# Kernel tuning notes

Hardware: AMD Instinct MI355X
Metric: run time of the kernel (lower is better)

The kernel has to match this reference:

```python
import jax, jax.numpy as jnp
from jax import lax
import numpy as np

VGG_C = 512
INNER = 32


def _conv3x3(x, w, b):
    # x: [B,C,H,W], w: [O,I,3,3], padding=1 (SAME)
    y = lax.conv_general_dilated(x, w, (1, 1), 'SAME',
                                 dimension_numbers=('NCHW', 'OIHW', 'NCHW'))
    return y + b[None, :, None, None]


def _predict_filter(style, cw, cb, fw, fb):
    # FilterPredictor_S: conv 512->32, global mean pool, FC 32 -> 9*32*32
    s = _conv3x3(style, cw, cb)                     # [B,32,H,W]
    pooled = s.mean(axis=(2, 3))                    # [B,32]
    f = pooled @ fw.T + fb                          # [B,9216]
    return f.reshape(-1, INNER, INNER, 3, 3)        # [B,outC,inC,3,3]


def _apply_filter(x, filt):
    # per-sample dynamic 3x3 conv: x [B,32,H,W], filt [B,32,32,3,3]
    def one(xi, wi):
        return lax.conv_general_dilated(xi[None], wi, (1, 1), 'SAME',
                                        dimension_numbers=('NCHW', 'OIHW', 'NCHW'))[0]
    return jax.vmap(one)(x, filt)


def setup_inputs() -> dict:
    key = jax.random.key(0)
    ks = jax.random.split(key, 16)
    B, H, W = 8, 64, 64
    sc = 0.02
    d = {
        'content': jax.random.normal(ks[0], (B, VGG_C, H, W), jnp.float32),
        'style': jax.random.normal(ks[1], (B, VGG_C, H, W), jnp.float32),
        'ds_w': jax.random.normal(ks[2], (INNER, VGG_C, 3, 3), jnp.float32) * sc,
        'ds_b': jnp.zeros((INNER,), jnp.float32),
        'up_w': jax.random.normal(ks[3], (VGG_C, INNER, 3, 3), jnp.float32) * sc,
        'up_b': jnp.zeros((VGG_C,), jnp.float32),
        'f1_cw': jax.random.normal(ks[4], (INNER, VGG_C, 3, 3), jnp.float32) * sc,
        'f1_cb': jnp.zeros((INNER,), jnp.float32),
        'f1_fw': jax.random.normal(ks[5], (9 * INNER * INNER, INNER), jnp.float32) * sc,
        'f1_fb': jnp.zeros((9 * INNER * INNER,), jnp.float32),
        'f2_cw': jax.random.normal(ks[6], (INNER, VGG_C, 3, 3), jnp.float32) * sc,
        'f2_cb': jnp.zeros((INNER,), jnp.float32),
        'f2_fw': jax.random.normal(ks[7], (9 * INNER * INNER, INNER), jnp.float32) * sc,
        'f2_fb': jnp.zeros((9 * INNER * INNER,), jnp.float32),
    }
    return d


def reference(content, style, ds_w, ds_b, up_w, up_b,
              f1_cw, f1_cb, f1_fw, f1_fb,
              f2_cw, f2_cb, f2_fw, f2_fb):
    c = _conv3x3(content, ds_w, ds_b)                       # [B,32,H,W]
    filt1 = _predict_filter(style, f1_cw, f1_cb, f1_fw, f1_fb)
    c = _apply_filter(c, filt1)
    c = jnp.where(c >= 0, c, 0.2 * c)                       # LeakyReLU(0.2)
    filt2 = _predict_filter(style, f2_cw, f2_cb, f2_fw, f2_fb)
    c = _apply_filter(c, filt2)
    return content + _conv3x3(c, up_w, up_b)
```

## Files before the change

kernel.cpp:

```cpp
#include <hip/hip_runtime.h>
#include <hip/hip_bf16.h>

#define NB 8
#define NC 512
#define HW 4096
#define INNER 32

typedef unsigned short u16;
typedef unsigned int u32;
typedef __attribute__((ext_vector_type(8))) short bf16x8;
typedef __attribute__((ext_vector_type(4))) float f32x4;

__device__ __forceinline__ float b2f(u16 u) {
    union { u32 a; float f; } z;
    z.a = ((u32)u) << 16;
    return z.f;
}

__device__ __forceinline__ u16 f2b(float v) {
    u32 x = __float_as_uint(v);
    return (u16)((x + 0x7fffu + ((x >> 16) & 1u)) >> 16);
}

__device__ __forceinline__ float ldin(const void* p, int idx, int isf32) {
    if (isf32) return ((const float*)p)[idx];
    return b2f(((const u16*)p)[idx]);
}

__device__ __forceinline__ void gld_lds16(const void* g, void* l) {
    __builtin_amdgcn_global_load_lds(
        (const __attribute__((address_space(1))) unsigned int*)g,
        (__attribute__((address_space(3))) unsigned int*)l, 16, 0, 0);
}

__device__ __forceinline__ int resolve_isf32(int hisf, const void* content) {
    if (hisf >= 0) return hisf;
    int lane = threadIdx.x & 63;
    u16 u = ((const u16*)content)[lane * 2048];
    int e = (u >> 7) & 0xff;
    unsigned long long m = __ballot(e >= 100 && e <= 150);
    return (__popcll(m) < 32) ? 1 : 0;
}


__device__ __forceinline__ void role_style(int bc, const void* style, float* S,
                                           int isf32, float* smf) {
    int base = bc * HW;
    int tid = threadIdx.x;
    float t = 0.f, top = 0.f, bot = 0.f, lft = 0.f, rgt = 0.f;
    for (int e = tid; e < HW; e += 256) {
        float v = ldin(style, base + e, isf32);
        int h = e >> 6, w = e & 63;
        t += v;
        top += (h == 0)  ? v : 0.f;
        bot += (h == 63) ? v : 0.f;
        lft += (w == 0)  ? v : 0.f;
        rgt += (w == 63) ? v : 0.f;
    }
#pragma unroll
    for (int off = 32; off > 0; off >>= 1) {
        t   += __shfl_down(t, off);
        top += __shfl_down(top, off);
        bot += __shfl_down(bot, off);
        lft += __shfl_down(lft, off);
        rgt += __shfl_down(rgt, off);
    }
    int wave = tid >> 6;
    if ((tid & 63) == 0) {
        smf[wave * 5 + 0] = t; smf[wave * 5 + 1] = top; smf[wave * 5 + 2] = bot;
        smf[wave * 5 + 3] = lft; smf[wave * 5 + 4] = rgt;
    }
    __syncthreads();
    if (tid == 0) {
        t   = smf[0] + smf[5] + smf[10] + smf[15];
        top = smf[1] + smf[6] + smf[11] + smf[16];
        bot = smf[2] + smf[7] + smf[12] + smf[17];
        lft = smf[3] + smf[8] + smf[13] + smf[18];
        rgt = smf[4] + smf[9] + smf[14] + smf[19];
        float c00 = ldin(style, base + 0,    isf32);
        float c0W = ldin(style, base + 63,   isf32);
        float cH0 = ldin(style, base + 4032, isf32);
        float cHW = ldin(style, base + 4095, isf32);
        float* o = S + bc * 9;
        o[0] = t - bot - rgt + cHW;
        o[1] = t - bot;
        o[2] = t - bot - lft + cH0;
        o[3] = t - rgt;
        o[4] = t;
        o[5] = t - lft;
        o[6] = t - top - rgt + c0W;
        o[7] = t - top;
        o[8] = t - top - lft + c00;
    }
}

__device__ __forceinline__ void role_transform(int ridx, const void* content,
        u16* cT, int bstart, int isf32, float* lds) {
    int h  = ridx & 63;
    int ci = (ridx >> 6) & 15;
    int b4 = ridx >> 10;
    int tid = threadIdx.x;
    size_t gbase = ((size_t)(bstart + b4) * NC + ci * 32) * HW + (size_t)h * 64;
    if (isf32) {
#pragma unroll
        for (int k = 0; k < 2; k++) {
            int q = tid + k * 256;
            int c = q >> 4, w0 = (q & 15) * 4;
            float4 v = *(const float4*)((const float*)content + gbase + (size_t)c * HW + w0);
            lds[c * 65 + w0 + 0] = v.x;
            lds[c * 65 + w0 + 1] = v.y;
            lds[c * 65 + w0 + 2] = v.z;
            lds[c * 65 + w0 + 3] = v.w;
        }
    } else {
        int c = tid >> 3, w0 = (tid & 7) * 8;
        uint4 v = *(const uint4*)((const u16*)content + gbase + (size_t)c * HW + w0);
        lds[c * 65 + w0 + 0] = b2f((u16)(v.x & 0xffffu));
        lds[c * 65 + w0 + 1] = b2f((u16)(v.x >> 16));
        lds[c * 65 + w0 + 2] = b2f((u16)(v.y & 0xffffu));
        lds[c * 65 + w0 + 3] = b2f((u16)(v.y >> 16));
        lds[c * 65 + w0 + 4] = b2f((u16)(v.z & 0xffffu));
        lds[c * 65 + w0 + 5] = b2f((u16)(v.z >> 16));
        lds[c * 65 + w0 + 6] = b2f((u16)(v.w & 0xffffu));
        lds[c * 65 + w0 + 7] = b2f((u16)(v.w >> 16));
    }
    __syncthreads();
    u32* out = (u32*)(cT + ((size_t)(b4 * 16 + ci) * 4096 + h * 64) * 32);
#pragma unroll
    for (int k = 0; k < 4; k++) {
        int j = tid + k * 256;
        int w = j >> 4, cpair = j & 15;
        int key = (w + 1) & 3;
        int p0 = cpair << 1;
        int lc = (((p0 >> 3) ^ key) << 3) | (p0 & 7);
        u32 v = (u32)f2b(lds[lc * 65 + w]) | ((u32)f2b(lds[(lc + 1) * 65 + w]) << 16);
        out[j] = v;
    }
}

__device__ __forceinline__ void role_prep_wdown(int ridx, const void* dsw,
        u16* Bp, int isf32) {
    int idx = ridx * 256 + threadIdx.x;
    int e = idx & 7, l = (idx >> 3) & 63, nf = (idx >> 9) & 1;
    int cb = (idx >> 10) & 15, t9 = idx >> 14;
    int oc = nf * 16 + (l & 15);
    int c = cb * 32 + (l >> 4) * 8 + e;
    Bp[idx] = f2b(ldin(dsw, (oc * NC + c) * 9 + t9, isf32));
}

__device__ __forceinline__ void role_prep_wup(int ridx, const void* upw,
        u16* B2p, int isf32) {
    int idx = ridx * 256 + threadIdx.x;
    int e = idx & 7, l = (idx >> 3) & 63, nfo = (idx >> 9) & 31, t9 = idx >> 14;
    int oc = nfo * 16 + (l & 15);
    int ic = (l >> 4) * 8 + e;
    B2p[idx] = f2b(ldin(upw, (oc * INNER + ic) * 9 + t9, isf32));
}

__device__ __forceinline__ void role_fc(int ridx, const float* pooled,
        const void* fw1, const void* fb1, const void* fw2, const void* fb2,
        u16* fpack, int isf32, float* p) {
    int set = ridx / 288;
    int rr = ridx - set * 288;
    int b = rr / 36;
    int chunk = rr - b * 36;
    int row = chunk * 256 + threadIdx.x;
    const void* fw = set ? fw2 : fw1;
    const void* fb = set ? fb2 : fb1;
    if (threadIdx.x < 32) p[threadIdx.x] = pooled[(set * NB + b) * 32 + threadIdx.x];
    __syncthreads();
    float acc = ldin(fb, row, isf32);
    if (isf32) {
        const float* fwf = (const float*)fw + row * 32;
#pragma unroll
        for (int j = 0; j < 32; j++) acc += fwf[j] * p[j];
    } else {
        const u32* w32 = (const u32*)((const u16*)fw + row * 32);
#pragma unroll
        for (int j = 0; j < 16; j++) {
            u32 u = w32[j];
            acc += b2f((u16)(u & 0xffffu)) * p[2 * j];
            acc += b2f((u16)(u >> 16)) * p[2 * j + 1];
        }
    }
    int oc = row / 288;
    int rem = row - oc * 288;
    int ic = rem / 9;
    int t9 = rem - ic * 9;
    int l = (oc & 15) | ((ic >> 3) << 4);
    int e = ic & 7;
    int nf = oc >> 4;
    fpack[((((set * NB + b) * 9 + t9) * 2 + nf) * 64 + l) * 8 + e] = f2b(acc);
}

__device__ __forceinline__ void role_conv_down(int x, const u16* cT,
        const u16* Bp, const void* dsb, u16* c0T, int bstart, int isf32,
        u16* lds) {
    u32* lds32 = (u32*)lds;
    int b4 = x >> 6, row = x & 63;
    int b = bstart + b4;
    int tid = threadIdx.x, lane = tid & 63;
    int wid = __builtin_amdgcn_readfirstlane(tid >> 6);
    for (int i = tid; i < 3 * 66 * 16; i += 256) lds32[i] = 0u;
    __syncthreads();

    int m = lane & 15, g = lane >> 4;
    int wbase = wid * 16;
    f32x4 acc0 = {0.f, 0.f, 0.f, 0.f}, acc1 = {0.f, 0.f, 0.f, 0.f};

    for (int ci = 0; ci < 16; ci++) {
        if (ci) __syncthreads();
        const u16* sp = cT + ((size_t)(b4 * 16 + ci) * 4096) * 32;
#pragma unroll
        for (int r = 0; r < 3; r++) {
            int gh = row + r - 1;
            if (gh >= 0 && gh < 64)
                gld_lds16(sp + (size_t)gh * 2048 + tid * 8,
                          (char*)lds + (r * 66 + 1) * 64 + wid * 1024);
        }
        __syncthreads();
#pragma unroll
        for (int t9 = 0; t9 < 9; t9++) {
            int dh = t9 / 3, dw = t9 - dh * 3;
            int wi = wbase + m + dw;
            bf16x8 a = *(const bf16x8*)(lds + ((dh * 66 + wi) * 32 + ((g ^ (wi & 3)) * 8)));
            bf16x8 b0 = ((const bf16x8*)Bp)[((t9 * 16 + ci) * 2 + 0) * 64 + lane];
            bf16x8 b1 = ((const bf16x8*)Bp)[((t9 * 16 + ci) * 2 + 1) * 64 + lane];
            acc0 = __builtin_amdgcn_mfma_f32_16x16x32_bf16(a, b0, acc0, 0, 0, 0);
            acc1 = __builtin_amdgcn_mfma_f32_16x16x32_bf16(a, b1, acc1, 0, 0, 0);
        }
    }
    float bia0 = ldin(dsb, m, isf32);
    float bia1 = ldin(dsb, 16 + m, isf32);
    size_t obase = ((size_t)b * 4096 + row * 64) * 32;
    int pix0 = wbase + g * 4;
#pragma unroll
    for (int r = 0; r < 4; r++) {
        int w = pix0 + r;
        int key = (w + 1) & 3;
        int p0 = (((m >> 3) ^ key) << 3) | (m & 7);
        int p1 = ((((16 + m) >> 3) ^ key) << 3) | (m & 7);
        c0T[obase + (size_t)w * 32 + p0] = f2b(acc0[r] + bia0);
        c0T[obase + (size_t)w * 32 + p1] = f2b(acc1[r] + bia1);
    }
}

__device__ __forceinline__ void role_pooled(int p, const float* S,
        const void* cw1, const void* cb1, const void* cw2, const void* cb2,
        float* pooled, int isf32) {
    int tid = threadIdx.x;
    int pair = p * 4 + (tid >> 6);
    int set = pair >> 8;
    int rem = pair & 255;
    int b = rem >> 5;
    int o = rem & 31;
    const void* cw = set ? cw2 : cw1;
    const void* cb = set ? cb2 : cb1;
    int lane = tid & 63;
    float acc = 0.f;
    const float* Sb = S + b * NC * 9;
    int wbase = o * NC * 9;
    for (int c = lane; c < NC; c += 64) {
#pragma unroll
        for (int k = 0; k < 9; k++)
            acc += Sb[c * 9 + k] * ldin(cw, wbase + c * 9 + k, isf32);
    }
#pragma unroll
    for (int off = 32; off > 0; off >>= 1) acc += __shfl_down(acc, off);
    if (lane == 0)
        pooled[(set * NB + b) * INNER + o] = acc * (1.0f / 4096.0f) + ldin(cb, o, isf32);
}


__global__ __launch_bounds__(256) void k_front(
        const void* __restrict__ style, float* __restrict__ S, int nStyle,
        const void* __restrict__ content, u16* __restrict__ cT, int bstart, int nT,
        const void* __restrict__ dsw, u16* __restrict__ Bp,
        const void* __restrict__ upw, u16* __restrict__ B2p, int nPrep,
        const float* __restrict__ pooled,
        const void* __restrict__ fw1, const void* __restrict__ fb1,
        const void* __restrict__ fw2, const void* __restrict__ fb2,
        u16* __restrict__ fpack, int hisf) {
    __shared__ float smf[32 * 65];
    int isf32 = resolve_isf32(hisf, content);
    int x = blockIdx.x;
    if (x < nStyle) { role_style(x, style, S, isf32, smf); return; }
    x -= nStyle;
    if (x < nT) { role_transform(x, content, cT, bstart, isf32, smf); return; }
    x -= nT;
    if (x < nPrep) { role_prep_wdown(x, dsw, Bp, isf32); return; }
    x -= nPrep;
    if (x < nPrep) { role_prep_wup(x, upw, B2p, isf32); return; }
    x -= nPrep;
    role_fc(x, pooled, fw1, fb1, fw2, fb2, fpack, isf32, smf);
}

__global__ __launch_bounds__(256) void k_mid(
        const u16* __restrict__ cT, const u16* __restrict__ Bp,
        const void* __restrict__ dsb, u16* __restrict__ c0T, int bstart, int nCD,
        const float* __restrict__ S,
        const void* __restrict__ cw1, const void* __restrict__ cb1,
        const void* __restrict__ cw2, const void* __restrict__ cb2,
        float* __restrict__ pooled, const void* __restrict__ content, int hisf) {
    __shared__ u16 lds[3 * 66 * 32];
    int isf32 = resolve_isf32(hisf, content);
    int x = blockIdx.x;
    if (x < nCD) { role_conv_down(x, cT, Bp, dsb, c0T, bstart, isf32, lds); return; }
    role_pooled(x - nCD, S, cw1, cb1, cw2, cb2, pooled, isf32);
}

__global__ __launch_bounds__(256) void k_apply(const u16* __restrict__ srcT,
        const u16* __restrict__ fpack, u16* __restrict__ dstT, int lrelu) {
    int b = blockIdx.x >> 6, row = blockIdx.x & 63;
    int tid = threadIdx.x, lane = tid & 63;
    int wid = __builtin_amdgcn_readfirstlane(tid >> 6);
    __shared__ u16 lds[3 * 66 * 32];
    u32* lds32 = (u32*)lds;
    for (int i = tid; i < 96; i += 256) {
        int r = i >> 5, side = (i >> 4) & 1, cpr = i & 15;
        lds32[(r * 66 + side * 65) * 16 + cpr] = 0u;
    }
    const u16* sp = srcT + (size_t)b * 64 * 64 * 32;
    for (int r = 0; r < 3; r++) {
        int gh = row + r - 1;
        u32 ldsoff = (u32)(r * 66 + 1) * 64 + (u32)wid * 1024;
        if (gh >= 0 && gh < 64) {
            gld_lds16(sp + (size_t)gh * 2048 + tid * 8, (char*)lds + ldsoff);
        } else {
            int4 z = make_int4(0, 0, 0, 0);
            *(int4*)((char*)lds + ldsoff + (u32)lane * 16) = z;
        }
    }
    __syncthreads();

    int m = lane & 15, g = lane >> 4, wbase = wid * 16;
    f32x4 acc0 = {0.f, 0.f, 0.f, 0.f}, acc1 = {0.f, 0.f, 0.f, 0.f};
    const bf16x8* FB = (const bf16x8*)fpack + (size_t)b * 1152;
#pragma unroll
    for (int t9 = 0; t9 < 9; t9++) {
        int dh = t9 / 3, dw = t9 - dh * 3;
        int wi = wbase + m + dw;
        bf16x8 a = *(const bf16x8*)(lds + ((dh * 66 + wi) * 32 + ((g ^ (wi & 3)) * 8)));
        bf16x8 b0 = FB[(t9 * 2 + 0) * 64 + lane];
        bf16x8 b1 = FB[(t9 * 2 + 1) * 64 + lane];
        acc0 = __builtin_amdgcn_mfma_f32_16x16x32_bf16(a, b0, acc0, 0, 0, 0);
        acc1 = __builtin_amdgcn_mfma_f32_16x16x32_bf16(a, b1, acc1, 0, 0, 0);
    }
    size_t obase = ((size_t)(b * 64 + row) * 64) * 32;
    int pix0 = wbase + g * 4;
#pragma unroll
    for (int r = 0; r < 4; r++) {
        float v0 = acc0[r], v1 = acc1[r];
        if (lrelu) {
            v0 = (v0 >= 0.f) ? v0 : 0.2f * v0;
            v1 = (v1 >= 0.f) ? v1 : 0.2f * v1;
        }
        int w = pix0 + r;
        int key = (w + 1) & 3;
        int p0 = (((m >> 3) ^ key) << 3) | (m & 7);
        int p1 = ((((16 + m) >> 3) ^ key) << 3) | (m & 7);
        dstT[obase + (size_t)w * 32 + p0] = f2b(v0);
        dstT[obase + (size_t)w * 32 + p1] = f2b(v1);
    }
}

__global__ __launch_bounds__(256) void k_conv_up(const u16* __restrict__ c2T,
        const u16* __restrict__ B2p, const void* __restrict__ upb,
        const void* __restrict__ content, void* __restrict__ outv, int hisf) {
    int isf32 = resolve_isf32(hisf, content);
    int b = blockIdx.x >> 6, row = blockIdx.x & 63;
    int nq = blockIdx.y;
    int tid = threadIdx.x, lane = tid & 63;
    int wid = __builtin_amdgcn_readfirstlane(tid >> 6);
    __shared__ char smem[64 * 68 * 4] __attribute__((aligned(16)));
    u16* lds = (u16*)smem;
    u32* lds32 = (u32*)smem;
    for (int i = tid; i < 96; i += 256) {
        int r = i >> 5, side = (i >> 4) & 1, cpr = i & 15;
        lds32[(r * 66 + side * 65) * 16 + cpr] = 0u;
    }
    const u16* sp = c2T + (size_t)b * 64 * 64 * 32;
    for (int r = 0; r < 3; r++) {
        int gh = row + r - 1;
        u32 ldsoff = (u32)(r * 66 + 1) * 64 + (u32)wid * 1024;
        if (gh >= 0 && gh < 64) {
            gld_lds16(sp + (size_t)gh * 2048 + tid * 8, (char*)lds + ldsoff);
        } else {
            int4 z = make_int4(0, 0, 0, 0);
            *(int4*)((char*)lds + ldsoff + (u32)lane * 16) = z;
        }
    }
    __syncthreads();

    int m = lane & 15, g = lane >> 4, wbase = wid * 16;
    f32x4 acc[8];
#pragma unroll
    for (int i = 0; i < 8; i++) acc[i] = (f32x4){0.f, 0.f, 0.f, 0.f};
#pragma unroll
    for (int t9 = 0; t9 < 9; t9++) {
        int dh = t9 / 3, dw = t9 - dh * 3;
        int wi = wbase + m + dw;
        bf16x8 a = *(const bf16x8*)(lds + ((dh * 66 + wi) * 32 + ((g ^ (wi & 3)) * 8)));
#pragma unroll
        for (int nfl = 0; nfl < 8; nfl++) {
            bf16x8 bw = ((const bf16x8*)B2p)[(t9 * 32 + nq * 8 + nfl) * 64 + lane];
            acc[nfl] = __builtin_amdgcn_mfma_f32_16x16x32_bf16(a, bw, acc[nfl], 0, 0, 0);
        }
    }

    int pix0 = wbase + g * 4;
    float* fl = (float*)smem;
    int ocl2 = tid >> 4;
    int px0 = (tid & 15) * 4;
    __syncthreads();
#pragma unroll
    for (int hf = 0; hf < 2; hf++) {
        if (hf) __syncthreads();
#pragma unroll
        for (int nf = 0; nf < 4; nf++) {
            int ocl = nf * 16 + m;
            *(f32x4*)(fl + ocl * 68 + pix0) = acc[hf * 4 + nf];
        }
        __syncthreads();
#pragma unroll
        for (int p = 0; p < 4; p++) {
            int ocl = p * 16 + ocl2;
            int oc = nq * 128 + hf * 64 + ocl;
            float bias = ldin(upb, oc, isf32);
            f32x4 v4 = *(const f32x4*)(fl + ocl * 68 + px0);
            size_t idx = ((size_t)b * NC + oc) * HW + (size_t)row * 64 + px0;
            if (isf32) {
                f32x4 rsd = *(const f32x4*)((const float*)content + idx);
                f32x4 ov;
#pragma unroll
                for (int r = 0; r < 4; r++) ov[r] = v4[r] + bias + rsd[r];
                *(f32x4*)((float*)outv + idx) = ov;
            } else {
                ushort4 rv = *(const ushort4*)((const u16*)content + idx);
                ushort4 ov;
                ov.x = f2b(v4[0] + bias + b2f(rv.x));
                ov.y = f2b(v4[1] + bias + b2f(rv.y));
                ov.z = f2b(v4[2] + bias + b2f(rv.z));
                ov.w = f2b(v4[3] + bias + b2f(rv.w));
                *(ushort4*)((u16*)outv + idx) = ov;
            }
        }
    }
}

extern "C" void kernel_launch(void* const* d_in, const int* in_sizes, int n_in,
                              void* d_out, int out_size, void* d_ws, size_t ws_size,
                              hipStream_t stream) {
    const void* content = d_in[0];
    const void* style   = d_in[1];
    const void* ds_w    = d_in[2];
    const void* ds_b    = d_in[3];
    const void* up_w    = d_in[4];
    const void* up_b    = d_in[5];
    const void* f1_cw   = d_in[6];
    const void* f1_cb   = d_in[7];
    const void* f1_fw   = d_in[8];
    const void* f1_fb   = d_in[9];
    const void* f2_cw   = d_in[10];
    const void* f2_cb   = d_in[11];
    const void* f2_fw   = d_in[12];
    const void* f2_fb   = d_in[13];

    int hisf = -1;
    if (in_sizes && n_in >= 1) {
        if (in_sizes[0] == NB * NC * HW * 4) hisf = 1;
        else if (in_sizes[0] == NB * NC * HW * 2) hisf = 0;
    }

    const size_t SZ_PACK = 294912;
    const size_t SZ_CT2  = 2097152;
    const size_t REQ_WS  = 3 * SZ_CT2 + 3 * SZ_PACK + 147456 * 4 + 2048 + 64;

    if (ws_size >= REQ_WS) {
        char* w = (char*)d_ws;
        u16*   B2pack = (u16*)w;                 w += SZ_PACK;
        u16*   c2T    = (u16*)w;                 w += SZ_CT2;
        u16*   c0T    = (u16*)w;                 w += SZ_CT2;
        u16*   c1T    = (u16*)w;                 w += SZ_CT2;
        u16*   Bpack  = (u16*)w;                 w += SZ_PACK;
        u16*   fpack  = (u16*)w;                 w += SZ_PACK;
        float* S      = (float*)w;               w += 147456 * 4;
        float* pooled = (float*)w;
        u16*   cT     = (u16*)d_out;

        k_front<<<4096 + 8192 + 2 * 576, 256, 0, stream>>>(
            style, S, 4096, content, cT, 0, 8192,
            ds_w, Bpack, up_w, B2pack, 576,
            pooled, f1_fw, f1_fb, f2_fw, f2_fb, fpack, hisf);
        k_mid<<<512 + 128, 256, 0, stream>>>(
            cT, Bpack, ds_b, c0T, 0, 512,
            S, f1_cw, f1_cb, f2_cw, f2_cb, pooled, content, hisf);
        k_front<<<576, 256, 0, stream>>>(
            style, S, 0, content, cT, 0, 0,
            ds_w, Bpack, up_w, B2pack, 0,
            pooled, f1_fw, f1_fb, f2_fw, f2_fb, fpack, hisf);
        k_apply<<<NB * 64, 256, 0, stream>>>(c0T, fpack, c1T, 1);
        k_apply<<<NB * 64, 256, 0, stream>>>(c1T, fpack + NB * 9216, c2T, 0);
        k_conv_up<<<dim3(NB * 64, 4), 256, 0, stream>>>(c2T, B2pack, up_b,
                                                        content, d_out, hisf);
    } else {
        float* S      = (float*)d_out;
        float* pooled = S + 36864;
        u16*   fpack  = (u16*)(pooled + 512);
        u16*   Bpack  = fpack + 147456;
        u16*   c0T    = Bpack + 147456;
        u16*   c1T    = c0T + 1048576;
        u16*   cTh    = c1T + 1048576;
        u16*   B2pack = (u16*)d_ws;
        u16*   c2T    = B2pack + 147456;

        k_front<<<4096 + 4096 + 2 * 576, 256, 0, stream>>>(
            style, S, 4096, content, cTh, 0, 4096,
            ds_w, Bpack, up_w, B2pack, 576,
            pooled, f1_fw, f1_fb, f2_fw, f2_fb, fpack, hisf);
        k_mid<<<256 + 128, 256, 0, stream>>>(
            cTh, Bpack, ds_b, c0T, 0, 256,
            S, f1_cw, f1_cb, f2_cw, f2_cb, pooled, content, hisf);
        k_front<<<4096 + 576, 256, 0, stream>>>(
            style, S, 0, content, cTh, 4, 4096,
            ds_w, Bpack, up_w, B2pack, 0,
            pooled, f1_fw, f1_fb, f2_fw, f2_fb, fpack, hisf);
        k_mid<<<256, 256, 0, stream>>>(
            cTh, Bpack, ds_b, c0T, 4, 256,
            S, f1_cw, f1_cb, f2_cw, f2_cb, pooled, content, hisf);
        k_apply<<<NB * 64, 256, 0, stream>>>(c0T, fpack, c1T, 1);
        k_apply<<<NB * 64, 256, 0, stream>>>(c1T, fpack + NB * 9216, c2T, 0);
        k_conv_up<<<dim3(NB * 64, 4), 256, 0, stream>>>(c2T, B2pack, up_b,
                                                        content, d_out, hisf);
    }
}
```

Measured before the change: 283.6 us.

## Fuse style pooling conv into style blocks via atomics, drop extra FC launch

Each style block now projects its nine shifted-window sums through both predictor conv weights and atomically accumulates into a raw pooled buffer. This removes the S intermediate and the separate pooled role, and moves the FC role into k_mid, which cuts one kernel launch. The style reduction is vectorised, and the transform role now handles two rows per block to halve its block count. In exchange it adds a memset and atomic contention, and the float summation order now varies from run to run.

```diff
diff --git a/kernel.cpp b/kernel.cpp
--- a/kernel.cpp
+++ b/kernel.cpp
@@ -43,19 +43,45 @@
 }
 
 
-__device__ __forceinline__ void role_style(int bc, const void* style, float* S,
-                                           int isf32, float* smf) {
+__device__ __forceinline__ void role_style(int bc, const void* style,
+        const void* cw1, const void* cw2, float* pooled_raw,
+        int isf32, float* smf) {
+    int b = bc >> 9, c = bc & 511;
     int base = bc * HW;
     int tid = threadIdx.x;
     float t = 0.f, top = 0.f, bot = 0.f, lft = 0.f, rgt = 0.f;
-    for (int e = tid; e < HW; e += 256) {
-        float v = ldin(style, base + e, isf32);
-        int h = e >> 6, w = e & 63;
-        t += v;
-        top += (h == 0)  ? v : 0.f;
-        bot += (h == 63) ? v : 0.f;
-        lft += (w == 0)  ? v : 0.f;
-        rgt += (w == 63) ? v : 0.f;
+    if (isf32) {
+        const float4* sp = (const float4*)((const float*)style + base);
+#pragma unroll
+        for (int k = 0; k < 4; k++) {
+            int q = tid + k * 256;
+            float4 v = sp[q];
+            float s4 = (v.x + v.y) + (v.z + v.w);
+            int h = q >> 4, w0 = (q & 15) * 4;
+            t += s4;
+            if (h == 0)   top += s4;
+            if (h == 63)  bot += s4;
+            if (w0 == 0)  lft += v.x;
+            if (w0 == 60) rgt += v.w;
+        }
+    } else {
+        const uint4* sp = (const uint4*)((const u16*)style + base);
+#pragma unroll
+        for (int k = 0; k < 2; k++) {
+            int q = tid + k * 256;
+            uint4 v = sp[q];
+            float e0 = b2f((u16)(v.x & 0xffffu)), e1 = b2f((u16)(v.x >> 16));
+            float e2 = b2f((u16)(v.y & 0xffffu)), e3 = b2f((u16)(v.y >> 16));
+            float e4 = b2f((u16)(v.z & 0xffffu)), e5 = b2f((u16)(v.z >> 16));
+            float e6 = b2f((u16)(v.w & 0xffffu)), e7 = b2f((u16)(v.w >> 16));
+            float s8 = ((e0 + e1) + (e2 + e3)) + ((e4 + e5) + (e6 + e7));
+            int h = q >> 3, w0 = (q & 7) * 8;
+            t += s8;
+            if (h == 0)   top += s8;
+            if (h == 63)  bot += s8;
+            if (w0 == 0)  lft += e0;
+            if (w0 == 56) rgt += e7;
+        }
     }
 #pragma unroll
     for (int off = 32; off > 0; off >>= 1) {
@@ -67,74 +93,95 @@
     }
     int wave = tid >> 6;
     if ((tid & 63) == 0) {
-        smf[wave * 5 + 0] = t; smf[wave * 5 + 1] = top; smf[wave * 5 + 2] = bot;
-        smf[wave * 5 + 3] = lft; smf[wave * 5 + 4] = rgt;
+        smf[20 + wave * 5 + 0] = t;   smf[20 + wave * 5 + 1] = top;
+        smf[20 + wave * 5 + 2] = bot; smf[20 + wave * 5 + 3] = lft;
+        smf[20 + wave * 5 + 4] = rgt;
     }
     __syncthreads();
     if (tid == 0) {
-        t   = smf[0] + smf[5] + smf[10] + smf[15];
-        top = smf[1] + smf[6] + smf[11] + smf[16];
-        bot = smf[2] + smf[7] + smf[12] + smf[17];
-        lft = smf[3] + smf[8] + smf[13] + smf[18];
-        rgt = smf[4] + smf[9] + smf[14] + smf[19];
+        t   = smf[20] + smf[25] + smf[30] + smf[35];
+        top = smf[21] + smf[26] + smf[31] + smf[36];
+        bot = smf[22] + smf[27] + smf[32] + smf[37];
+        lft = smf[23] + smf[28] + smf[33] + smf[38];
+        rgt = smf[24] + smf[29] + smf[34] + smf[39];
         float c00 = ldin(style, base + 0,    isf32);
         float c0W = ldin(style, base + 63,   isf32);
         float cH0 = ldin(style, base + 4032, isf32);
         float cHW = ldin(style, base + 4095, isf32);
-        float* o = S + bc * 9;
-        o[0] = t - bot - rgt + cHW;
-        o[1] = t - bot;
-        o[2] = t - bot - lft + cH0;
-        o[3] = t - rgt;
-        o[4] = t;
-        o[5] = t - lft;
-        o[6] = t - top - rgt + c0W;
-        o[7] = t - top;
-        o[8] = t - top - lft + c00;
+        smf[0] = t - bot - rgt + cHW;
+        smf[1] = t - bot;
+        smf[2] = t - bot - lft + cH0;
+        smf[3] = t - rgt;
+        smf[4] = t;
+        smf[5] = t - lft;
+        smf[6] = t - top - rgt + c0W;
+        smf[7] = t - top;
+        smf[8] = t - top - lft + c00;
+    }
+    __syncthreads();
+    if (tid < 64) {
+        int set = tid >> 5, o = tid & 31;
+        const void* cw = set ? cw2 : cw1;
+        int wb = (o * NC + c) * 9;
+        float acc = 0.f;
+#pragma unroll
+        for (int k = 0; k < 9; k++) acc += ldin(cw, wb + k, isf32) * smf[k];
+        atomicAdd(&pooled_raw[(set * NB + b) * 32 + o], acc);
     }
 }
 
 __device__ __forceinline__ void role_transform(int ridx, const void* content,
         u16* cT, int bstart, int isf32, float* lds) {
-    int h  = ridx & 63;
-    int ci = (ridx >> 6) & 15;
-    int b4 = ridx >> 10;
+    int hp = ridx & 31;
+    int ci = (ridx >> 5) & 15;
+    int b4 = ridx >> 9;
     int tid = threadIdx.x;
-    size_t gbase = ((size_t)(bstart + b4) * NC + ci * 32) * HW + (size_t)h * 64;
+    size_t gbase = ((size_t)(bstart + b4) * NC + ci * 32) * HW + (size_t)hp * 128;
     if (isf32) {
 #pragma unroll
-        for (int k = 0; k < 2; k++) {
-            int q = tid + k * 256;
-            int c = q >> 4, w0 = (q & 15) * 4;
-            float4 v = *(const float4*)((const float*)content + gbase + (size_t)c * HW + w0);
-            lds[c * 65 + w0 + 0] = v.x;
-            lds[c * 65 + w0 + 1] = v.y;
-            lds[c * 65 + w0 + 2] = v.z;
-            lds[c * 65 + w0 + 3] = v.w;
-        }
+        for (int r2 = 0; r2 < 2; r2++)
+#pragma unroll
+            for (int k = 0; k < 2; k++) {
+                int q = tid + k * 256;
+                int c = q >> 4, w0 = (q & 15) * 4;
+                float4 v = *(const float4*)((const float*)content
+                            + gbase + (size_t)c * HW + r2 * 64 + w0);
+                float* dst = lds + r2 * 2080 + c * 65 + w0;
+                dst[0] = v.x; dst[1] = v.y; dst[2] = v.z; dst[3] = v.w;
+            }
     } else {
-        int c = tid >> 3, w0 = (tid & 7) * 8;
-        uint4 v = *(const uint4*)((const u16*)content + gbase + (size_t)c * HW + w0);
-        lds[c * 65 + w0 + 0] = b2f((u16)(v.x & 0xffffu));
-        lds[c * 65 + w0 + 1] = b2f((u16)(v.x >> 16));
-        lds[c * 65 + w0 + 2] = b2f((u16)(v.y & 0xffffu));
-        lds[c * 65 + w0 + 3] = b2f((u16)(v.y >> 16));
-        lds[c * 65 + w0 + 4] = b2f((u16)(v.z & 0xffffu));
-        lds[c * 65 + w0 + 5] = b2f((u16)(v.z >> 16));
-        lds[c * 65 + w0 + 6] = b2f((u16)(v.w & 0xffffu));
-        lds[c * 65 + w0 + 7] = b2f((u16)(v.w >> 16));
-    }
-    __syncthreads();
-    u32* out = (u32*)(cT + ((size_t)(b4 * 16 + ci) * 4096 + h * 64) * 32);
-#pragma unroll
-    for (int k = 0; k < 4; k++) {
-        int j = tid + k * 256;
-        int w = j >> 4, cpair = j & 15;
-        int key = (w + 1) & 3;
-        int p0 = cpair << 1;
-        int lc = (((p0 >> 3) ^ key) << 3) | (p0 & 7);
-        u32 v = (u32)f2b(lds[lc * 65 + w]) | ((u32)f2b(lds[(lc + 1) * 65 + w]) << 16);
-        out[j] = v;
+#pragma unroll
+        for (int r2 = 0; r2 < 2; r2++) {
+            int c = tid >> 3, w0 = (tid & 7) * 8;
+            uint4 v = *(const uint4*)((const u16*)content
+                        + gbase + (size_t)c * HW + r2 * 64 + w0);
+            float* dst = lds + r2 * 2080 + c * 65 + w0;
+            dst[0] = b2f((u16)(v.x & 0xffffu));
+            dst[1] = b2f((u16)(v.x >> 16));
+            dst[2] = b2f((u16)(v.y & 0xffffu));
+            dst[3] = b2f((u16)(v.y >> 16));
+            dst[4] = b2f((u16)(v.z & 0xffffu));
+            dst[5] = b2f((u16)(v.z >> 16));
+            dst[6] = b2f((u16)(v.w & 0xffffu));
+            dst[7] = b2f((u16)(v.w >> 16));
+        }
+    }
+    __syncthreads();
+#pragma unroll
+    for (int r2 = 0; r2 < 2; r2++) {
+        u32* out = (u32*)(cT + ((size_t)(b4 * 16 + ci) * 4096
+                                + (hp * 2 + r2) * 64) * 32);
+        const float* src = lds + r2 * 2080;
+#pragma unroll
+        for (int k = 0; k < 4; k++) {
+            int j = tid + k * 256;
+            int w = j >> 4, cpair = j & 15;
+            int key = (w + 1) & 3;
+            int p0 = cpair << 1;
+            int lc = (((p0 >> 3) ^ key) << 3) | (p0 & 7);
+            out[j] = (u32)f2b(src[lc * 65 + w])
+                   | ((u32)f2b(src[(lc + 1) * 65 + w]) << 16);
+        }
     }
 }
 
@@ -157,7 +204,8 @@
     B2p[idx] = f2b(ldin(upw, (oc * INNER + ic) * 9 + t9, isf32));
 }
 
-__device__ __forceinline__ void role_fc(int ridx, const float* pooled,
+__device__ __forceinline__ void role_fc(int ridx, const float* pooled_raw,
+        const void* cbf1, const void* cbf2,
         const void* fw1, const void* fb1, const void* fw2, const void* fb2,
         u16* fpack, int isf32, float* p) {
     int set = ridx / 288;
@@ -167,7 +215,10 @@
     int row = chunk * 256 + threadIdx.x;
     const void* fw = set ? fw2 : fw1;
     const void* fb = set ? fb2 : fb1;
-    if (threadIdx.x < 32) p[threadIdx.x] = pooled[(set * NB + b) * 32 + threadIdx.x];
+    if (threadIdx.x < 32)
+        p[threadIdx.x] = pooled_raw[(set * NB + b) * 32 + threadIdx.x]
+                           * (1.0f / 4096.0f)
+                       + ldin(set ? cbf2 : cbf1, threadIdx.x, isf32);
     __syncthreads();
     float acc = ldin(fb, row, isf32);
     if (isf32) {
@@ -245,68 +296,41 @@
     }
 }
 
-__device__ __forceinline__ void role_pooled(int p, const float* S,
-        const void* cw1, const void* cb1, const void* cw2, const void* cb2,
-        float* pooled, int isf32) {
-    int tid = threadIdx.x;
-    int pair = p * 4 + (tid >> 6);
-    int set = pair >> 8;
-    int rem = pair & 255;
-    int b = rem >> 5;
-    int o = rem & 31;
-    const void* cw = set ? cw2 : cw1;
-    const void* cb = set ? cb2 : cb1;
-    int lane = tid & 63;
-    float acc = 0.f;
-    const float* Sb = S + b * NC * 9;
-    int wbase = o * NC * 9;
-    for (int c = lane; c < NC; c += 64) {
-#pragma unroll
-        for (int k = 0; k < 9; k++)
-            acc += Sb[c * 9 + k] * ldin(cw, wbase + c * 9 + k, isf32);
-    }
-#pragma unroll
-    for (int off = 32; off > 0; off >>= 1) acc += __shfl_down(acc, off);
-    if (lane == 0)
-        pooled[(set * NB + b) * INNER + o] = acc * (1.0f / 4096.0f) + ldin(cb, o, isf32);
-}
-
 
 __global__ __launch_bounds__(256) void k_front(
-        const void* __restrict__ style, float* __restrict__ S, int nStyle,
+        const void* __restrict__ style,
+        const void* __restrict__ cw1, const void* __restrict__ cw2,
+        float* __restrict__ pooled_raw, int nStyle,
         const void* __restrict__ content, u16* __restrict__ cT, int bstart, int nT,
         const void* __restrict__ dsw, u16* __restrict__ Bp,
         const void* __restrict__ upw, u16* __restrict__ B2p, int nPrep,
-        const float* __restrict__ pooled,
-        const void* __restrict__ fw1, const void* __restrict__ fb1,
-        const void* __restrict__ fw2, const void* __restrict__ fb2,
-        u16* __restrict__ fpack, int hisf) {
-    __shared__ float smf[32 * 65];
+        int hisf) {
+    __shared__ float smf[2 * 2080];
     int isf32 = resolve_isf32(hisf, content);
     int x = blockIdx.x;
-    if (x < nStyle) { role_style(x, style, S, isf32, smf); return; }
+    if (x < nStyle) { role_style(x, style, cw1, cw2, pooled_raw, isf32, smf); return; }
     x -= nStyle;
     if (x < nT) { role_transform(x, content, cT, bstart, isf32, smf); return; }
     x -= nT;
     if (x < nPrep) { role_prep_wdown(x, dsw, Bp, isf32); return; }
     x -= nPrep;
-    if (x < nPrep) { role_prep_wup(x, upw, B2p, isf32); return; }
-    x -= nPrep;
-    role_fc(x, pooled, fw1, fb1, fw2, fb2, fpack, isf32, smf);
+    role_prep_wup(x, upw, B2p, isf32);
 }
 
 __global__ __launch_bounds__(256) void k_mid(
         const u16* __restrict__ cT, const u16* __restrict__ Bp,
         const void* __restrict__ dsb, u16* __restrict__ c0T, int bstart, int nCD,
-        const float* __restrict__ S,
-        const void* __restrict__ cw1, const void* __restrict__ cb1,
-        const void* __restrict__ cw2, const void* __restrict__ cb2,
-        float* __restrict__ pooled, const void* __restrict__ content, int hisf) {
+        const float* __restrict__ pooled_raw,
+        const void* __restrict__ cbf1, const void* __restrict__ cbf2,
+        const void* __restrict__ fw1, const void* __restrict__ fb1,
+        const void* __restrict__ fw2, const void* __restrict__ fb2,
+        u16* __restrict__ fpack, const void* __restrict__ content, int hisf) {
     __shared__ u16 lds[3 * 66 * 32];
     int isf32 = resolve_isf32(hisf, content);
     int x = blockIdx.x;
     if (x < nCD) { role_conv_down(x, cT, Bp, dsb, c0T, bstart, isf32, lds); return; }
-    role_pooled(x - nCD, S, cw1, cb1, cw2, cb2, pooled, isf32);
+    role_fc(x - nCD, pooled_raw, cbf1, cbf2, fw1, fb1, fw2, fb2, fpack,
+            isf32, (float*)lds);
 }
 
 __global__ __launch_bounds__(256) void k_apply(const u16* __restrict__ srcT,
@@ -474,7 +498,7 @@
 
     const size_t SZ_PACK = 294912;
     const size_t SZ_CT2  = 2097152;
-    const size_t REQ_WS  = 3 * SZ_CT2 + 3 * SZ_PACK + 147456 * 4 + 2048 + 64;
+    const size_t REQ_WS  = 3 * SZ_CT2 + 3 * SZ_PACK + 2048 + 64;
 
     if (ws_size >= REQ_WS) {
         char* w = (char*)d_ws;
@@ -484,29 +508,25 @@
         u16*   c1T    = (u16*)w;                 w += SZ_CT2;
         u16*   Bpack  = (u16*)w;                 w += SZ_PACK;
         u16*   fpack  = (u16*)w;                 w += SZ_PACK;
-        float* S      = (float*)w;               w += 147456 * 4;
-        float* pooled = (float*)w;
+        float* pooled_raw = (float*)w;
         u16*   cT     = (u16*)d_out;
 
-        k_front<<<4096 + 8192 + 2 * 576, 256, 0, stream>>>(
-            style, S, 4096, content, cT, 0, 8192,
-            ds_w, Bpack, up_w, B2pack, 576,
-            pooled, f1_fw, f1_fb, f2_fw, f2_fb, fpack, hisf);
-        k_mid<<<512 + 128, 256, 0, stream>>>(
+        hipMemsetAsync(pooled_raw, 0, 2 * NB * 32 * 4, stream);
+        k_front<<<4096 + 4096 + 2 * 576, 256, 0, stream>>>(
+            style, f1_cw, f2_cw, pooled_raw, 4096,
+            content, cT, 0, 4096,
+            ds_w, Bpack, up_w, B2pack, 576, hisf);
+        k_mid<<<512 + 576, 256, 0, stream>>>(
             cT, Bpack, ds_b, c0T, 0, 512,
-            S, f1_cw, f1_cb, f2_cw, f2_cb, pooled, content, hisf);
-        k_front<<<576, 256, 0, stream>>>(
-            style, S, 0, content, cT, 0, 0,
-            ds_w, Bpack, up_w, B2pack, 0,
-            pooled, f1_fw, f1_fb, f2_fw, f2_fb, fpack, hisf);
+            pooled_raw, f1_cb, f2_cb,
+            f1_fw, f1_fb, f2_fw, f2_fb, fpack, content, hisf);
         k_apply<<<NB * 64, 256, 0, stream>>>(c0T, fpack, c1T, 1);
         k_apply<<<NB * 64, 256, 0, stream>>>(c1T, fpack + NB * 9216, c2T, 0);
         k_conv_up<<<dim3(NB * 64, 4), 256, 0, stream>>>(c2T, B2pack, up_b,
                                                         content, d_out, hisf);
     } else {
-        float* S      = (float*)d_out;
-        float* pooled = S + 36864;
-        u16*   fpack  = (u16*)(pooled + 512);
+        float* pooled_raw = (float*)d_out;
+        u16*   fpack  = (u16*)(pooled_raw + 512);
         u16*   Bpack  = fpack + 147456;
         u16*   c0T    = Bpack + 147456;
         u16*   c1T    = c0T + 1048576;
@@ -514,20 +534,23 @@
         u16*   B2pack = (u16*)d_ws;
         u16*   c2T    = B2pack + 147456;
 
-        k_front<<<4096 + 4096 + 2 * 576, 256, 0, stream>>>(
-            style, S, 4096, content, cTh, 0, 4096,
-            ds_w, Bpack, up_w, B2pack, 576,
-            pooled, f1_fw, f1_fb, f2_fw, f2_fb, fpack, hisf);
-        k_mid<<<256 + 128, 256, 0, stream>>>(
+        hipMemsetAsync(pooled_raw, 0, 2 * NB * 32 * 4, stream);
+        k_front<<<4096 + 2048 + 2 * 576, 256, 0, stream>>>(
+            style, f1_cw, f2_cw, pooled_raw, 4096,
+            content, cTh, 0, 2048,
+            ds_w, Bpack, up_w, B2pack, 576, hisf);
+        k_mid<<<256 + 576, 256, 0, stream>>>(
             cTh, Bpack, ds_b, c0T, 0, 256,
-            S, f1_cw, f1_cb, f2_cw, f2_cb, pooled, content, hisf);
-        k_front<<<4096 + 576, 256, 0, stream>>>(
-            style, S, 0, content, cTh, 4, 4096,
-            ds_w, Bpack, up_w, B2pack, 0,
-            pooled, f1_fw, f1_fb, f2_fw, f2_fb, fpack, hisf);
+            pooled_raw, f1_cb, f2_cb,
+            f1_fw, f1_fb, f2_fw, f2_fb, fpack, content, hisf);
+        k_front<<<2048, 256, 0, stream>>>(
+            style, f1_cw, f2_cw, pooled_raw, 0,
+            content, cTh, 4, 2048,
+            ds_w, Bpack, up_w, B2pack, 0, hisf);
         k_mid<<<256, 256, 0, stream>>>(
             cTh, Bpack, ds_b, c0T, 4, 256,
-            S, f1_cw, f1_cb, f2_cw, f2_cb, pooled, content, hisf);
+            pooled_raw, f1_cb, f2_cb,
+            f1_fw, f1_fb, f2_fw, f2_fb, fpack, content, hisf);
         k_apply<<<NB * 64, 256, 0, stream>>>(c0T, fpack, c1T, 1);
         k_apply<<<NB * 64, 256, 0, stream>>>(c1T, fpack + NB * 9216, c2T, 0);
         k_conv_up<<<dim3(NB * 64, 4), 256, 0, stream>>>(c2T, B2pack, up_b,
```

Result: no change. 283.7 us (+0.0%).
